# Performance work log

Hardware: AMD Instinct MI355X
Metric: run time of the kernel (lower is better)

## Reference

```python
import jax, jax.numpy as jnp
import numpy as np

N, T, D = 64, 4096, 128


def setup_inputs() -> dict:
    key = jax.random.key(0)
    k1, k2, k3, k4 = jax.random.split(key, 4)
    return {
        "query": jax.random.normal(k1, (N, D), dtype=jnp.float32),
        "key": jax.random.normal(k2, (T, N, D), dtype=jnp.float32),
        "value": jax.random.normal(k3, (T, N, D), dtype=jnp.float32),
        "speech_len": jax.random.randint(k4, (N,), 0, T, dtype=jnp.int64),
    }


def reference(query, key, value, speech_len):
    # energy[n, t] = <key[t, n, :], query[n, :]>   (torch: bmm(key^T, q).squeeze)
    energy = jnp.einsum("tnd,nd->nt", key, query)  # (N, T)
    # per-row length mask: mask[i, :speech_len[i]] = 1
    t_idx = jnp.arange(energy.shape[1])
    mask = (t_idx[None, :] < speech_len[:, None]).astype(energy.dtype)  # (N, T)
    # faithful to source: multiplicative mask (zeros energy, NOT -inf)
    score = jax.nn.softmax(mask * energy, axis=1)
    # redundant renormalization kept for faithfulness
    score = score / jnp.sum(score, axis=1, keepdims=True)
    # context[n, v] = sum_t score[n, t] * value[t, n, v]
    context = jnp.einsum("nt,tnv->nv", score, value)  # (N, D)
    return context, mask
```

## Files before the change

kernel.cpp:

```cpp
#include <hip/hip_runtime.h>

#define N_  64
#define T_  4096
#define D_  128
#define CH_ 32
#define TC_ (T_ / CH_)

__global__ __launch_bounds__(256) void energy_kernel(const float* __restrict__ key,
                                                     const float* __restrict__ query,
                                                     float* __restrict__ energy) {
    const int lane = threadIdx.x & 63;
    const int wave = threadIdx.x >> 6;
    const int n  = blockIdx.x >> 6;
    const int t0 = ((blockIdx.x & 63) << 6) + (wave << 4);

    const float2 q = *reinterpret_cast<const float2*>(query + n * D_ + lane * 2);

    #pragma unroll 4
    for (int i = 0; i < 16; ++i) {
        const int t = t0 + i;
        const float2 k2 = *reinterpret_cast<const float2*>(
            key + ((size_t)t * N_ + n) * D_ + lane * 2);
        float p = k2.x * q.x + k2.y * q.y;
        #pragma unroll
        for (int off = 32; off; off >>= 1) p += __shfl_xor(p, off, 64);
        if (lane == 0) energy[n * T_ + t] = p;
    }
}

__global__ __launch_bounds__(256) void softmax_kernel(float* __restrict__ energy_score,
                                                      const int* __restrict__ slen,
                                                      float* __restrict__ mask_out) {
    const int n   = blockIdx.x;
    const int len = slen[n];
    const int tid = threadIdx.x;
    const int lane = tid & 63;
    const int wv   = tid >> 6;

    float ev[T_ / 256];
    #pragma unroll
    for (int i = 0; i < T_ / 256; ++i) {
        const int t = tid + i * 256;
        const float e = energy_score[n * T_ + t];
        ev[i] = (t < len) ? e : 0.f;
    }

    float m = -3.4e38f;
    #pragma unroll
    for (int i = 0; i < T_ / 256; ++i) m = fmaxf(m, ev[i]);
    #pragma unroll
    for (int off = 32; off; off >>= 1) m = fmaxf(m, __shfl_xor(m, off, 64));
    __shared__ float wred[4];
    if (lane == 0) wred[wv] = m;
    __syncthreads();
    m = fmaxf(fmaxf(wred[0], wred[1]), fmaxf(wred[2], wred[3]));
    __syncthreads();

    float s = 0.f;
    #pragma unroll
    for (int i = 0; i < T_ / 256; ++i) s += __expf(ev[i] - m);
    #pragma unroll
    for (int off = 32; off; off >>= 1) s += __shfl_xor(s, off, 64);
    if (lane == 0) wred[wv] = s;
    __syncthreads();
    s = wred[0] + wred[1] + wred[2] + wred[3];
    const float inv = 1.f / s;

    #pragma unroll
    for (int i = 0; i < T_ / 256; ++i) {
        const int t = tid + i * 256;
        energy_score[n * T_ + t] = __expf(ev[i] - m) * inv;
        mask_out[n * T_ + t] = (t < len) ? 1.f : 0.f;
    }
}

__global__ __launch_bounds__(256) void ctx_partial_kernel(const float* __restrict__ value,
                                                          const float* __restrict__ score,
                                                          float* __restrict__ part) {
    const int n = blockIdx.x / CH_;
    const int c = blockIdx.x % CH_;
    const int lane = threadIdx.x & 63;
    const int g    = threadIdx.x >> 6;
    const int tbase = c * TC_;

    float2 acc = make_float2(0.f, 0.f);
    for (int i = g; i < TC_; i += 4) {
        const int t = tbase + i;
        const float sc = score[n * T_ + t];
        const float2 v2 = *reinterpret_cast<const float2*>(
            value + ((size_t)t * N_ + n) * D_ + lane * 2);
        acc.x += sc * v2.x;
        acc.y += sc * v2.y;
    }

    __shared__ float2 red[4][64];
    red[g][lane] = acc;
    __syncthreads();
    if (g == 0) {
        const float2 a = red[0][lane], b = red[1][lane];
        const float2 cc = red[2][lane], d = red[3][lane];
        float2 r;
        r.x = (a.x + b.x) + (cc.x + d.x);
        r.y = (a.y + b.y) + (cc.y + d.y);
        *reinterpret_cast<float2*>(part + ((size_t)(n * CH_ + c)) * D_ + lane * 2) = r;
    }
}

__global__ __launch_bounds__(128) void ctx_reduce_kernel(const float* __restrict__ part,
                                                         float* __restrict__ ctx_out) {
    const int n = blockIdx.x;
    const int v = threadIdx.x;
    float acc = 0.f;
    #pragma unroll 8
    for (int c = 0; c < CH_; ++c) acc += part[((size_t)(n * CH_ + c)) * D_ + v];
    ctx_out[n * D_ + v] = acc;
}

extern "C" void kernel_launch(void* const* d_in, const int* in_sizes, int n_in,
                              void* d_out, int out_size, void* d_ws, size_t ws_size,
                              hipStream_t stream) {
    const float* query = (const float*)d_in[0];
    const float* key   = (const float*)d_in[1];
    const float* value = (const float*)d_in[2];
    const int*   slen  = (const int*)d_in[3];

    float* out      = (float*)d_out;
    float* ctx_out  = out;
    float* mask_out = out + N_ * D_;

    float* energy_score = (float*)d_ws;
    float* partials     = energy_score + N_ * T_;

    energy_kernel<<<N_ * (T_ / 64), 256, 0, stream>>>(key, query, energy_score);
    softmax_kernel<<<N_, 256, 0, stream>>>(energy_score, slen, mask_out);
    ctx_partial_kernel<<<N_ * CH_, 256, 0, stream>>>(value, energy_score, partials);
    ctx_reduce_kernel<<<N_, 128, 0, stream>>>(partials, ctx_out);
}
```

Measured before the change: 288.8 us.

## Fuse energy, softmax and context into one split-softmax chunk kernel

Replaces the four-kernel pipeline with a single chunked kernel that, per (row, time-chunk), computes the energies, a local max and exp-sum, and the weighted value accumulation. A small finalize kernel then merges the chunks with online-softmax rescaling. This removes the global energy/score round trip and two launches, and widens loads to float4. The trade-off is extra exp rescaling work and less parallelism inside each block, since only 128 of the 256 threads take part in the softmax step.

```diff
diff --git a/kernel.cpp b/kernel.cpp
--- a/kernel.cpp
+++ b/kernel.cpp
@@ -6,114 +6,122 @@
 #define CH_ 32
 #define TC_ (T_ / CH_)
 
-__global__ __launch_bounds__(256) void energy_kernel(const float* __restrict__ key,
-                                                     const float* __restrict__ query,
-                                                     float* __restrict__ energy) {
-    const int lane = threadIdx.x & 63;
-    const int wave = threadIdx.x >> 6;
-    const int n  = blockIdx.x >> 6;
-    const int t0 = ((blockIdx.x & 63) << 6) + (wave << 4);
+__global__ __launch_bounds__(256) void chunk_kernel(
+    const float* __restrict__ key, const float* __restrict__ value,
+    const float* __restrict__ query, const int* __restrict__ slen,
+    float* __restrict__ mask_out, float* __restrict__ m_ws,
+    float* __restrict__ s_ws, float* __restrict__ acc_ws)
+{
+    const int n    = blockIdx.x / CH_;
+    const int c    = blockIdx.x % CH_;
+    const int tid  = threadIdx.x;
+    const int lane = tid & 63;
+    const int wv   = tid >> 6;
+    const int half = lane >> 5;
+    const int hl   = lane & 31;
+    const int tbase = c * TC_;
+    const int len   = slen[n];
 
-    const float2 q = *reinterpret_cast<const float2*>(query + n * D_ + lane * 2);
+    __shared__ float  ep[TC_];
+    __shared__ float  wred[8];
+    __shared__ float4 red[4][32];
+
+    const float4 q4 = *reinterpret_cast<const float4*>(query + n * D_ + hl * 4);
 
     #pragma unroll 4
     for (int i = 0; i < 16; ++i) {
-        const int t = t0 + i;
-        const float2 k2 = *reinterpret_cast<const float2*>(
-            key + ((size_t)t * N_ + n) * D_ + lane * 2);
-        float p = k2.x * q.x + k2.y * q.y;
+        const int lt = wv * 32 + i * 2 + half;
+        const int t  = tbase + lt;
+        const float4 k4 = *reinterpret_cast<const float4*>(
+            key + ((size_t)t * N_ + n) * D_ + hl * 4);
+        float p = k4.x * q4.x + k4.y * q4.y + k4.z * q4.z + k4.w * q4.w;
         #pragma unroll
-        for (int off = 32; off; off >>= 1) p += __shfl_xor(p, off, 64);
-        if (lane == 0) energy[n * T_ + t] = p;
+        for (int off = 16; off; off >>= 1) p += __shfl_xor(p, off, 64);
+        if (hl == 0) ep[lt] = (t < len) ? p : 0.f;
+    }
+    __syncthreads();
+
+    const float ev = (tid < TC_) ? ep[tid] : -3.4e38f;
+    float m = ev;
+    #pragma unroll
+    for (int off = 32; off; off >>= 1) m = fmaxf(m, __shfl_xor(m, off, 64));
+    if (lane == 0) wred[wv] = m;
+    __syncthreads();
+    m = fmaxf(fmaxf(wred[0], wred[1]), fmaxf(wred[2], wred[3]));
+
+    float sp = 0.f;
+    if (tid < TC_) {
+        const float p = __expf(ev - m);
+        ep[tid] = p;
+        sp = p;
+        mask_out[n * T_ + tbase + tid] = (tbase + tid < len) ? 1.f : 0.f;
+    }
+    #pragma unroll
+    for (int off = 32; off; off >>= 1) sp += __shfl_xor(sp, off, 64);
+    if (lane == 0) wred[4 + wv] = sp;
+    __syncthreads();
+    if (tid == 0) {
+        m_ws[n * CH_ + c] = m;
+        s_ws[n * CH_ + c] = wred[4] + wred[5] + wred[6] + wred[7];
+    }
+
+    float4 acc = make_float4(0.f, 0.f, 0.f, 0.f);
+    #pragma unroll 4
+    for (int i = 0; i < 16; ++i) {
+        const int lt = wv * 32 + i * 2 + half;
+        const int t  = tbase + lt;
+        const float4 v4 = *reinterpret_cast<const float4*>(
+            value + ((size_t)t * N_ + n) * D_ + hl * 4);
+        const float pv = ep[lt];
+        acc.x += pv * v4.x; acc.y += pv * v4.y;
+        acc.z += pv * v4.z; acc.w += pv * v4.w;
+    }
+    acc.x += __shfl_xor(acc.x, 32, 64);
+    acc.y += __shfl_xor(acc.y, 32, 64);
+    acc.z += __shfl_xor(acc.z, 32, 64);
+    acc.w += __shfl_xor(acc.w, 32, 64);
+    if (half == 0) red[wv][hl] = acc;
+    __syncthreads();
+    if (tid < 32) {
+        const float4 a = red[0][tid], b = red[1][tid];
+        const float4 e = red[2][tid], d = red[3][tid];
+        float4 r;
+        r.x = (a.x + b.x) + (e.x + d.x);
+        r.y = (a.y + b.y) + (e.y + d.y);
+        r.z = (a.z + b.z) + (e.z + d.z);
+        r.w = (a.w + b.w) + (e.w + d.w);
+        *reinterpret_cast<float4*>(acc_ws + ((size_t)(n * CH_ + c)) * D_ + tid * 4) = r;
     }
 }
 
-__global__ __launch_bounds__(256) void softmax_kernel(float* __restrict__ energy_score,
-                                                      const int* __restrict__ slen,
-                                                      float* __restrict__ mask_out) {
-    const int n   = blockIdx.x;
-    const int len = slen[n];
-    const int tid = threadIdx.x;
-    const int lane = tid & 63;
-    const int wv   = tid >> 6;
+__global__ __launch_bounds__(64) void finalize_kernel(
+    const float* __restrict__ m_ws, const float* __restrict__ s_ws,
+    const float* __restrict__ acc_ws, float* __restrict__ ctx)
+{
+    const int n    = blockIdx.x;
+    const int lane = threadIdx.x;
 
-    float ev[T_ / 256];
+    const float mc = (lane < CH_) ? m_ws[n * CH_ + lane] : -3.4e38f;
+    float M = mc;
     #pragma unroll
-    for (int i = 0; i < T_ / 256; ++i) {
-        const int t = tid + i * 256;
-        const float e = energy_score[n * T_ + t];
-        ev[i] = (t < len) ? e : 0.f;
+    for (int off = 32; off; off >>= 1) M = fmaxf(M, __shfl_xor(M, off, 64));
+
+    const float ew = (lane < CH_) ? __expf(mc - M) : 0.f;
+    float S = (lane < CH_) ? s_ws[n * CH_ + lane] * ew : 0.f;
+    #pragma unroll
+    for (int off = 32; off; off >>= 1) S += __shfl_xor(S, off, 64);
+
+    float2 r = make_float2(0.f, 0.f);
+    #pragma unroll 8
+    for (int c = 0; c < CH_; ++c) {
+        const float w = __shfl(ew, c, 64);
+        const float2 a = *reinterpret_cast<const float2*>(
+            acc_ws + ((size_t)(n * CH_ + c)) * D_ + lane * 2);
+        r.x += w * a.x; r.y += w * a.y;
     }
-
-    float m = -3.4e38f;
-    #pragma unroll
-    for (int i = 0; i < T_ / 256; ++i) m = fmaxf(m, ev[i]);
-    #pragma unroll
-    for (int off = 32; off; off >>= 1) m = fmaxf(m, __shfl_xor(m, off, 64));
-    __shared__ float wred[4];
-    if (lane == 0) wred[wv] = m;
-    __syncthreads();
-    m = fmaxf(fmaxf(wred[0], wred[1]), fmaxf(wred[2], wred[3]));
-    __syncthreads();
-
-    float s = 0.f;
-    #pragma unroll
-    for (int i = 0; i < T_ / 256; ++i) s += __expf(ev[i] - m);
-    #pragma unroll
-    for (int off = 32; off; off >>= 1) s += __shfl_xor(s, off, 64);
-    if (lane == 0) wred[wv] = s;
-    __syncthreads();
-    s = wred[0] + wred[1] + wred[2] + wred[3];
-    const float inv = 1.f / s;
-
-    #pragma unroll
-    for (int i = 0; i < T_ / 256; ++i) {
-        const int t = tid + i * 256;
-        energy_score[n * T_ + t] = __expf(ev[i] - m) * inv;
-        mask_out[n * T_ + t] = (t < len) ? 1.f : 0.f;
-    }
-}
-
-__global__ __launch_bounds__(256) void ctx_partial_kernel(const float* __restrict__ value,
-                                                          const float* __restrict__ score,
-                                                          float* __restrict__ part) {
-    const int n = blockIdx.x / CH_;
-    const int c = blockIdx.x % CH_;
-    const int lane = threadIdx.x & 63;
-    const int g    = threadIdx.x >> 6;
-    const int tbase = c * TC_;
-
-    float2 acc = make_float2(0.f, 0.f);
-    for (int i = g; i < TC_; i += 4) {
-        const int t = tbase + i;
-        const float sc = score[n * T_ + t];
-        const float2 v2 = *reinterpret_cast<const float2*>(
-            value + ((size_t)t * N_ + n) * D_ + lane * 2);
-        acc.x += sc * v2.x;
-        acc.y += sc * v2.y;
-    }
-
-    __shared__ float2 red[4][64];
-    red[g][lane] = acc;
-    __syncthreads();
-    if (g == 0) {
-        const float2 a = red[0][lane], b = red[1][lane];
-        const float2 cc = red[2][lane], d = red[3][lane];
-        float2 r;
-        r.x = (a.x + b.x) + (cc.x + d.x);
-        r.y = (a.y + b.y) + (cc.y + d.y);
-        *reinterpret_cast<float2*>(part + ((size_t)(n * CH_ + c)) * D_ + lane * 2) = r;
-    }
-}
-
-__global__ __launch_bounds__(128) void ctx_reduce_kernel(const float* __restrict__ part,
-                                                         float* __restrict__ ctx_out) {
-    const int n = blockIdx.x;
-    const int v = threadIdx.x;
-    float acc = 0.f;
-    #pragma unroll 8
-    for (int c = 0; c < CH_; ++c) acc += part[((size_t)(n * CH_ + c)) * D_ + v];
-    ctx_out[n * D_ + v] = acc;
+    const float invS = 1.f / S;
+    *reinterpret_cast<float2*>(ctx + n * D_ + lane * 2) =
+        make_float2(r.x * invS, r.y * invS);
 }
 
 extern "C" void kernel_launch(void* const* d_in, const int* in_sizes, int n_in,
@@ -128,11 +136,11 @@
     float* ctx_out  = out;
     float* mask_out = out + N_ * D_;
 
-    float* energy_score = (float*)d_ws;
-    float* partials     = energy_score + N_ * T_;
+    float* m_ws   = (float*)d_ws;
+    float* s_ws   = m_ws + N_ * CH_;
+    float* acc_ws = s_ws + N_ * CH_;
 
-    energy_kernel<<<N_ * (T_ / 64), 256, 0, stream>>>(key, query, energy_score);
-    softmax_kernel<<<N_, 256, 0, stream>>>(energy_score, slen, mask_out);
-    ctx_partial_kernel<<<N_ * CH_, 256, 0, stream>>>(value, energy_score, partials);
-    ctx_reduce_kernel<<<N_, 128, 0, stream>>>(partials, ctx_out);
+    chunk_kernel<<<N_ * CH_, 256, 0, stream>>>(key, value, query, slen,
+                                               mask_out, m_ws, s_ws, acc_ws);
+    finalize_kernel<<<N_, 64, 0, stream>>>(m_ws, s_ws, acc_ws, ctx_out);
 }
```

Measured after the change: 275.3 us. -4.7%, faster.

## Use float4 loads over batch pairs with batched loads in energy and PV kernels

Applied to the files above, without the earlier changes.

Energy and weighted-value kernels now have each wave cover two adjacent batch rows with float4 loads, so one wave reads 512 contiguous bytes per timestep. Eight rows are loaded into registers before being consumed, which raises memory-level parallelism. The length mask moves into the energy kernel, and the context partials now split time into 64 chunks to feed a deeper final reduction. The cost is higher register use and more partials to reduce.

```diff
diff --git a/kernel.cpp b/kernel.cpp
--- a/kernel.cpp
+++ b/kernel.cpp
@@ -3,117 +3,147 @@
 #define N_  64
 #define T_  4096
 #define D_  128
-#define CH_ 32
-#define TC_ (T_ / CH_)
 
-__global__ __launch_bounds__(256) void energy_kernel(const float* __restrict__ key,
-                                                     const float* __restrict__ query,
-                                                     float* __restrict__ energy) {
-    const int lane = threadIdx.x & 63;
-    const int wave = threadIdx.x >> 6;
-    const int n  = blockIdx.x >> 6;
-    const int t0 = ((blockIdx.x & 63) << 6) + (wave << 4);
+__global__ __launch_bounds__(256) void energy_kernel(
+    const float* __restrict__ key, const float* __restrict__ query,
+    const int* __restrict__ slen, float* __restrict__ energy)
+{
+    const int tid   = threadIdx.x;
+    const int lane  = tid & 63;
+    const int wv    = tid >> 6;
+    const int w     = blockIdx.x * 4 + wv;
+    const int npair = w & 31;
+    const int t0    = (w >> 5) << 4;
+    const int nl    = lane >> 5;
+    const int d4    = lane & 31;
+    const int n     = npair * 2 + nl;
+    const int len   = slen[n];
 
-    const float2 q = *reinterpret_cast<const float2*>(query + n * D_ + lane * 2);
+    const float4 q4 = *reinterpret_cast<const float4*>(query + n * D_ + d4 * 4);
+    const float* kbase = key + ((size_t)t0 * N_ + npair * 2) * D_ + lane * 4;
+    const size_t st = (size_t)N_ * D_;
 
-    #pragma unroll 4
-    for (int i = 0; i < 16; ++i) {
-        const int t = t0 + i;
-        const float2 k2 = *reinterpret_cast<const float2*>(
-            key + ((size_t)t * N_ + n) * D_ + lane * 2);
-        float p = k2.x * q.x + k2.y * q.y;
+    float4 kb[8];
+    #pragma unroll
+    for (int g = 0; g < 2; ++g) {
         #pragma unroll
-        for (int off = 32; off; off >>= 1) p += __shfl_xor(p, off, 64);
-        if (lane == 0) energy[n * T_ + t] = p;
+        for (int i = 0; i < 8; ++i)
+            kb[i] = *reinterpret_cast<const float4*>(kbase + (size_t)(g * 8 + i) * st);
+        #pragma unroll
+        for (int i = 0; i < 8; ++i) {
+            float p = kb[i].x * q4.x + kb[i].y * q4.y
+                    + kb[i].z * q4.z + kb[i].w * q4.w;
+            #pragma unroll
+            for (int off = 16; off; off >>= 1) p += __shfl_xor(p, off, 64);
+            const int t = t0 + g * 8 + i;
+            if (d4 == 0) energy[(size_t)n * T_ + t] = (t < len) ? p : 0.f;
+        }
     }
 }
 
-__global__ __launch_bounds__(256) void softmax_kernel(float* __restrict__ energy_score,
-                                                      const int* __restrict__ slen,
-                                                      float* __restrict__ mask_out) {
-    const int n   = blockIdx.x;
-    const int len = slen[n];
-    const int tid = threadIdx.x;
+__global__ __launch_bounds__(256) void softmax_kernel(
+    float* __restrict__ energy_score, const int* __restrict__ slen,
+    float* __restrict__ mask_out)
+{
+    const int n    = blockIdx.x;
+    const int len  = slen[n];
+    const int tid  = threadIdx.x;
     const int lane = tid & 63;
     const int wv   = tid >> 6;
 
     float ev[T_ / 256];
     #pragma unroll
-    for (int i = 0; i < T_ / 256; ++i) {
-        const int t = tid + i * 256;
-        const float e = energy_score[n * T_ + t];
-        ev[i] = (t < len) ? e : 0.f;
-    }
+    for (int i = 0; i < T_ / 256; ++i)
+        ev[i] = energy_score[(size_t)n * T_ + tid + i * 256];
 
     float m = -3.4e38f;
     #pragma unroll
     for (int i = 0; i < T_ / 256; ++i) m = fmaxf(m, ev[i]);
     #pragma unroll
     for (int off = 32; off; off >>= 1) m = fmaxf(m, __shfl_xor(m, off, 64));
-    __shared__ float wred[4];
+    __shared__ float wred[8];
     if (lane == 0) wred[wv] = m;
     __syncthreads();
     m = fmaxf(fmaxf(wred[0], wred[1]), fmaxf(wred[2], wred[3]));
-    __syncthreads();
 
     float s = 0.f;
     #pragma unroll
     for (int i = 0; i < T_ / 256; ++i) s += __expf(ev[i] - m);
     #pragma unroll
     for (int off = 32; off; off >>= 1) s += __shfl_xor(s, off, 64);
-    if (lane == 0) wred[wv] = s;
+    if (lane == 0) wred[4 + wv] = s;
     __syncthreads();
-    s = wred[0] + wred[1] + wred[2] + wred[3];
+    s = wred[4] + wred[5] + wred[6] + wred[7];
     const float inv = 1.f / s;
 
     #pragma unroll
     for (int i = 0; i < T_ / 256; ++i) {
         const int t = tid + i * 256;
-        energy_score[n * T_ + t] = __expf(ev[i] - m) * inv;
-        mask_out[n * T_ + t] = (t < len) ? 1.f : 0.f;
+        energy_score[(size_t)n * T_ + t] = __expf(ev[i] - m) * inv;
+        mask_out[(size_t)n * T_ + t] = (t < len) ? 1.f : 0.f;
     }
 }
 
-__global__ __launch_bounds__(256) void ctx_partial_kernel(const float* __restrict__ value,
-                                                          const float* __restrict__ score,
-                                                          float* __restrict__ part) {
-    const int n = blockIdx.x / CH_;
-    const int c = blockIdx.x % CH_;
-    const int lane = threadIdx.x & 63;
-    const int g    = threadIdx.x >> 6;
-    const int tbase = c * TC_;
+__global__ __launch_bounds__(256) void pv_kernel(
+    const float* __restrict__ value, const float* __restrict__ score,
+    float* __restrict__ part)
+{
+    const int b     = blockIdx.x;
+    const int npair = b & 31;
+    const int c     = b >> 5;
+    const int tid   = threadIdx.x;
+    const int lane  = tid & 63;
+    const int g     = tid >> 6;
+    const int nl    = lane >> 5;
+    const int d4    = lane & 31;
+    const int n     = npair * 2 + nl;
+    const int t0    = c * 64 + g * 16;
 
-    float2 acc = make_float2(0.f, 0.f);
-    for (int i = g; i < TC_; i += 4) {
-        const int t = tbase + i;
-        const float sc = score[n * T_ + t];
-        const float2 v2 = *reinterpret_cast<const float2*>(
-            value + ((size_t)t * N_ + n) * D_ + lane * 2);
-        acc.x += sc * v2.x;
-        acc.y += sc * v2.y;
+    const float* vbase = value + ((size_t)t0 * N_ + npair * 2) * D_ + lane * 4;
+    const size_t st = (size_t)N_ * D_;
+
+    float4 acc = make_float4(0.f, 0.f, 0.f, 0.f);
+    float4 vb[8];
+    #pragma unroll
+    for (int gg = 0; gg < 2; ++gg) {
+        #pragma unroll
+        for (int i = 0; i < 8; ++i)
+            vb[i] = *reinterpret_cast<const float4*>(vbase + (size_t)(gg * 8 + i) * st);
+        #pragma unroll
+        for (int i = 0; i < 8; ++i) {
+            const float sc = score[(size_t)n * T_ + t0 + gg * 8 + i];
+            acc.x += sc * vb[i].x; acc.y += sc * vb[i].y;
+            acc.z += sc * vb[i].z; acc.w += sc * vb[i].w;
+        }
     }
 
-    __shared__ float2 red[4][64];
+    __shared__ float4 red[4][64];
     red[g][lane] = acc;
     __syncthreads();
-    if (g == 0) {
-        const float2 a = red[0][lane], b = red[1][lane];
-        const float2 cc = red[2][lane], d = red[3][lane];
-        float2 r;
-        r.x = (a.x + b.x) + (cc.x + d.x);
-        r.y = (a.y + b.y) + (cc.y + d.y);
-        *reinterpret_cast<float2*>(part + ((size_t)(n * CH_ + c)) * D_ + lane * 2) = r;
+    if (tid < 64) {
+        const float4 a = red[0][tid], bb = red[1][tid];
+        const float4 cc = red[2][tid], dd = red[3][tid];
+        float4 r;
+        r.x = (a.x + bb.x) + (cc.x + dd.x);
+        r.y = (a.y + bb.y) + (cc.y + dd.y);
+        r.z = (a.z + bb.z) + (cc.z + dd.z);
+        r.w = (a.w + bb.w) + (cc.w + dd.w);
+        *reinterpret_cast<float4*>(part + ((size_t)b * 2 + (tid >> 5)) * D_
+                                        + (tid & 31) * 4) = r;
     }
 }
 
-__global__ __launch_bounds__(128) void ctx_reduce_kernel(const float* __restrict__ part,
-                                                         float* __restrict__ ctx_out) {
+__global__ __launch_bounds__(128) void ctx_reduce_kernel(
+    const float* __restrict__ part, float* __restrict__ ctx)
+{
     const int n = blockIdx.x;
-    const int v = threadIdx.x;
-    float acc = 0.f;
+    const int d = threadIdx.x;
+    const int npair = n >> 1, nl = n & 1;
+    float a = 0.f;
     #pragma unroll 8
-    for (int c = 0; c < CH_; ++c) acc += part[((size_t)(n * CH_ + c)) * D_ + v];
-    ctx_out[n * D_ + v] = acc;
+    for (int c = 0; c < 64; ++c)
+        a += part[(((size_t)c * 32 + npair) * 2 + nl) * D_ + d];
+    ctx[(size_t)n * D_ + d] = a;
 }
 
 extern "C" void kernel_launch(void* const* d_in, const int* in_sizes, int n_in,
@@ -129,10 +159,10 @@
     float* mask_out = out + N_ * D_;
 
     float* energy_score = (float*)d_ws;
-    float* partials     = energy_score + N_ * T_;
+    float* part         = energy_score + (size_t)N_ * T_;
 
-    energy_kernel<<<N_ * (T_ / 64), 256, 0, stream>>>(key, query, energy_score);
+    energy_kernel<<<2048, 256, 0, stream>>>(key, query, slen, energy_score);
     softmax_kernel<<<N_, 256, 0, stream>>>(energy_score, slen, mask_out);
-    ctx_partial_kernel<<<N_ * CH_, 256, 0, stream>>>(value, energy_score, partials);
-    ctx_reduce_kernel<<<N_, 128, 0, stream>>>(partials, ctx_out);
+    pv_kernel<<<2048, 256, 0, stream>>>(value, energy_score, part);
+    ctx_reduce_kernel<<<N_, 128, 0, stream>>>(part, ctx_out);
 }
```

Measured after the change: 290.5 us. Within noise of the previous version (+0.6%).
